# Performance work log

Measured on AMD Instinct MI355X. Metric: run time of the kernel, lower is better.

## Reference

```python
import jax, jax.numpy as jnp
import numpy as np

KS = 10       # kernel_size
OUT_N = 10    # pred_frames_num
DCT_N = 10
BN_INV = 1.0 / np.sqrt(1.0 + 1e-5)  # BN eval with running_mean=0, running_var=1


def _get_dct_matrix(N):
    k = np.arange(N)[:, None].astype(np.float64)
    i = np.arange(N)[None, :].astype(np.float64)
    w = np.full((N, 1), np.sqrt(2.0 / N))
    w[0, 0] = np.sqrt(1.0 / N)
    dct_m = w * np.cos(np.pi * (i + 0.5) * k / N)
    idct_m = np.linalg.inv(dct_m)
    return dct_m.astype(np.float32), idct_m.astype(np.float32)


def _conv1d(x, w):
    # x: [B, Cin, L], w: [Cout, Cin, K] -> [B, Cout, L-K+1]
    return jax.lax.conv_general_dilated(x, w, (1,), 'VALID',
                                        dimension_numbers=('NCH', 'OIH', 'NCH'))


def setup_inputs() -> dict:
    keys = iter(jax.random.split(jax.random.key(0), 32))
    def rn(shape, s=0.06):
        return (jax.random.normal(next(keys), shape, jnp.float32) * s)
    d = {}
    d['src'] = jax.random.normal(next(keys), (128, 50, 66), jnp.float32)
    d['convQ_w1'] = rn((256, 66, 6)); d['convQ_w2'] = rn((256, 256, 5))
    d['convK_w1'] = rn((256, 66, 6)); d['convK_w2'] = rn((256, 256, 5))
    d['gc1_w'] = rn((20, 256)); d['gc1_att'] = rn((66, 66)); d['gc1_b'] = rn((256,))
    d['bn1_g'] = 1.0 + rn((16896,), 0.1); d['bn1_b'] = rn((16896,), 0.1)
    d['gcb_w1'] = rn((12, 256, 256)); d['gcb_att1'] = rn((12, 66, 66)); d['gcb_b1'] = rn((12, 256))
    d['gcb_bn1_g'] = 1.0 + rn((12, 16896), 0.1); d['gcb_bn1_b'] = rn((12, 16896), 0.1)
    d['gcb_w2'] = rn((12, 256, 256)); d['gcb_att2'] = rn((12, 66, 66)); d['gcb_b2'] = rn((12, 256))
    d['gcb_bn2_g'] = 1.0 + rn((12, 16896), 0.1); d['gcb_bn2_b'] = rn((12, 16896), 0.1)
    d['gc7_w'] = rn((256, 20)); d['gc7_att'] = rn((66, 66)); d['gc7_b'] = rn((20,))
    return d


def reference(src, convQ_w1, convQ_w2, convK_w1, convK_w2,
              gc1_w, gc1_att, gc1_b, bn1_g, bn1_b,
              gcb_w1, gcb_att1, gcb_b1, gcb_bn1_g, gcb_bn1_b,
              gcb_w2, gcb_att2, gcb_b2, gcb_bn2_g, gcb_bn2_b,
              gc7_w, gc7_att, gc7_b):
    bs, input_n, F = src.shape  # [128, 50, 66]
    dct_np, idct_np = _get_dct_matrix(KS + OUT_N)
    dct_m = jnp.asarray(dct_np)
    idct_m = jnp.asarray(idct_np)

    src_t = jnp.transpose(src, (0, 2, 1))             # [bs, F, T]
    src_key = src_t[:, :, :input_n - OUT_N]           # [bs, F, 40]
    src_query = src_t[:, :, -KS:]                     # [bs, F, 10]

    vn = input_n - KS - OUT_N + 1                     # 31
    vl = KS + OUT_N                                   # 20
    idx = np.arange(vl)[None, :] + np.arange(vn)[:, None]   # [vn, vl]
    src_value = src[:, idx].reshape(bs * vn, vl, F)   # sliding windows
    src_value = jnp.matmul(dct_m[:DCT_N], src_value)  # [bs*vn, 10, F]
    src_value = src_value.reshape(bs, vn, DCT_N, F).transpose(0, 1, 3, 2).reshape(bs, vn, F * DCT_N)

    key = jax.nn.relu(_conv1d(jax.nn.relu(_conv1d(src_key / 1000.0, convK_w1)), convK_w2))    # [bs,256,31]
    query = jax.nn.relu(_conv1d(jax.nn.relu(_conv1d(src_query / 1000.0, convQ_w1)), convQ_w2))  # [bs,256,1]

    score = jnp.matmul(query.transpose(0, 2, 1), key) + 1e-15   # [bs,1,31]
    att = score / jnp.sum(score, axis=2, keepdims=True)
    dct_att = jnp.matmul(att, src_value)[:, 0].reshape(bs, F, DCT_N)  # [bs,66,10]

    idx2 = np.concatenate([np.arange(input_n - KS, input_n), np.full(OUT_N, input_n - 1)])
    input_gcn = src[:, idx2]                                   # [bs,20,66]
    dct_in = jnp.matmul(dct_m[:DCT_N], input_gcn).transpose(0, 2, 1)  # [bs,66,10]
    x = jnp.concatenate([dct_in, dct_att], axis=-1)            # [bs,66,20]

    def gconv(h, A, W, b):
        # support = h @ W ; out = A @ support + b
        return jnp.einsum('nm,bmf->bnf', A, h @ W) + b

    def bn(h, g, b):
        sh = h.shape
        return (h.reshape(sh[0], -1) * (g * BN_INV) + b).reshape(sh)

    y = jnp.tanh(bn(gconv(x, gc1_att, gc1_w, gc1_b), bn1_g, bn1_b))  # [bs,66,256]

    def block(y, p):
        w1, a1, b1, g1, be1, w2, a2, b2, g2, be2 = p
        h = jnp.tanh(bn(gconv(y, a1, w1, b1), g1, be1))
        h = jnp.tanh(bn(gconv(h, a2, w2, b2), g2, be2))
        return h + y, None

    y, _ = jax.lax.scan(block, y, (gcb_w1, gcb_att1, gcb_b1, gcb_bn1_g, gcb_bn1_b,
                                   gcb_w2, gcb_att2, gcb_b2, gcb_bn2_g, gcb_bn2_b))

    y = gconv(y, gc7_att, gc7_w, gc7_b) + x                    # [bs,66,20]
    out_gcn = jnp.matmul(idct_m[:, :DCT_N], y[:, :, :DCT_N].transpose(0, 2, 1))  # [bs,20,66]
    return out_gcn[:, :, None, :]                              # [bs,20,1,66] (itera=1)
```

## Files before the change

kernel.cpp:

```cpp
#include <hip/hip_runtime.h>
#include <hip/hip_bf16.h>


typedef __attribute__((ext_vector_type(8))) short short8;
typedef __attribute__((ext_vector_type(4))) float float4v;
typedef __attribute__((ext_vector_type(4))) unsigned uint4v;

#define BNI 0.9999950000374995f

__device__ __forceinline__ short f2bf(float x){
  unsigned u = __float_as_uint(x);
  unsigned r = (u + 0x7fff + ((u >> 16) & 1)) >> 16;
  return (short)r;
}
__device__ __forceinline__ unsigned pk2(float a, float b){
  return (unsigned)(unsigned short)f2bf(a) | ((unsigned)(unsigned short)f2bf(b) << 16);
}
__device__ __forceinline__ float tanh_f(float x){
  x = fminf(fmaxf(x, -9.f), 9.f);
  float e = __expf(2.f * x);
  return (e - 1.f) * __builtin_amdgcn_rcpf(e + 1.f);
}

__global__ __launch_bounds__(256) void k_prep(
    const float* __restrict__ wK1, const float* __restrict__ wQ1,
    const float* __restrict__ wK2, const float* __restrict__ wQ2,
    const float* __restrict__ gw1, const float* __restrict__ gw2,
    const float* __restrict__ gc1_w,
    const float* __restrict__ gc1_att, const float* __restrict__ att1,
    const float* __restrict__ att2, const float* __restrict__ gc7_att,
    const float* __restrict__ g0, const float* __restrict__ be0, const float* __restrict__ b0,
    const float* __restrict__ g1a, const float* __restrict__ be1a, const float* __restrict__ b1a,
    const float* __restrict__ g2a, const float* __restrict__ be2a, const float* __restrict__ b2a,
    float* __restrict__ dct, short* __restrict__ w1T, short* __restrict__ w2T,
    short* __restrict__ wgT, short* __restrict__ gc1wT, short* __restrict__ aG,
    unsigned* __restrict__ bnP)
{
  __shared__ short tle[64][72];
  int bid = blockIdx.x, tid = threadIdx.x;
  if (bid < 2){
    int t = bid*256 + tid;
    if (t < 400){
      int k = t / 20, i = t % 20;
      double w = (k == 0) ? sqrt(1.0/20.0) : sqrt(2.0/20.0);
      dct[t] = (float)(w * cos(3.14159265358979323846 * (i + 0.5) * k / 20.0));
    }
  } else if (bid < 1026){
    int idx = (bid-2)*256 + tid;
    int f = idx >> 9, k = idx & 511;
    float v = 0.f;
    if (k < 396){
      int h = k / 66, c = k - h*66;
      const float* s = (f < 256) ? wK1 : wQ1;
      v = s[((f & 255)*66 + c)*6 + h];
    }
    w1T[idx] = f2bf(v);
  } else if (bid < 3586){
    int idx = (bid-1026)*256 + tid;
    int f = idx / 1280, k = idx - f*1280;
    int h = k >> 8, c = k & 255;
    const float* s = (f < 256) ? wK2 : wQ2;
    w2T[idx] = f2bf(s[((f & 255)*256 + c)*5 + h]);
  } else if (bid < 3970){
    int q = bid - 3586;
    int l = q >> 4, sub = q & 15;
    int kt = (sub >> 2)*64, ft = (sub & 3)*64;
    const float* s = (l < 12) ? (gw1 + l*65536) : (gw2 + (l-12)*65536);
    int c = tid & 63, r4 = tid >> 6;
    #pragma unroll
    for (int p = 0; p < 16; p++){
      int k = p*4 + r4;
      tle[k][c] = f2bf(s[(kt + k)*256 + ft + c]);
    }
    __syncthreads();
    #pragma unroll
    for (int p = 0; p < 16; p++){
      int f = p*4 + r4;
      wgT[l*65536 + (ft + f)*256 + kt + c] = tle[c][f];
    }
  } else if (bid < 4002){
    int idx = (bid-3970)*256 + tid;
    int f = idx >> 5, k = idx & 31;
    gc1wT[idx] = f2bf(k < 20 ? gc1_w[k*256 + f] : 0.f);
  } else if (bid < 4782){
    int idx = (bid-4002)*256 + tid;
    int li = idx / 7680, r = idx - li*7680;
    int n = r / 96, m = r - n*96;
    const float* Af;
    if (li == 0) Af = gc1_att;
    else if (li == 25) Af = gc7_att;
    else if (li & 1) Af = att1 + ((li-1)>>1)*4356;
    else             Af = att2 + ((li-2)>>1)*4356;
    aG[idx] = f2bf((n < 66 && m < 66) ? Af[n*66 + m] : 0.f);
  } else {
    int idx = (bid-4782)*256 + tid;
    if (idx < 25*16896){
      int li = idx / 16896, r = idx - li*16896;
      int f = r & 255;
      const float *g, *be, *bi;
      if (li == 0){ g = g0; be = be0; bi = b0; }
      else {
        int l = (li - 1) >> 1;
        if (li & 1){ g = g1a + l*16896; be = be1a + l*16896; bi = b1a + l*256; }
        else       { g = g2a + l*16896; be = be2a + l*16896; bi = b2a + l*256; }
      }
      float sc = g[r] * BNI;
      float sh = bi[f] * sc + be[r];
      bnP[idx] = pk2(sc, sh);
    }
  }
}

__global__ __launch_bounds__(256) void k_conv1(const float* __restrict__ src,
    const short* __restrict__ w1T, short* __restrict__ kc1q){
  int b = blockIdx.x, ns = blockIdx.y;
  int f0 = ns*128;
  __shared__ short Aim[48*424];
  __shared__ short Wt[128*72];
  int tid = threadIdx.x;
  for (int idx = tid; idx < 48*424; idx += 256){
    int t = idx / 424, kk = idx - t*424;
    float v = 0.f;
    if (kk < 396 && t < 40){
      int h = kk / 66, c = kk - h*66;
      int row = t + h + ((t >= 35) ? 5 : 0);
      v = src[(b*50 + row)*66 + c] * 1e-3f;
    }
    Aim[idx] = f2bf(v);
  }
  int w = tid >> 6, lane = tid & 63, fl = lane & 15, g = lane >> 4;
  float4v acc[3][2];
  #pragma unroll
  for (int i=0;i<3;i++) for (int n=0;n<2;n++) acc[i][n] = (float4v){0.f,0.f,0.f,0.f};
  for (int kt = 0; kt < 416; kt += 64){
    __syncthreads();
    for (int ch = tid; ch < 128*8; ch += 256){
      int r = ch >> 3, kq = ch & 7;
      *(short8*)&Wt[r*72 + kq*8] = *(const short8*)&w1T[(f0 + r)*512 + kt + kq*8];
    }
    __syncthreads();
    int nst = (416 - kt >= 64) ? 2 : 1;
    for (int s = 0; s < nst; s++){
      int k0 = s*32;
      short8 bfr0 = *(const short8*)&Wt[(w*32 + fl)*72 + k0 + g*8];
      short8 bfr1 = *(const short8*)&Wt[(w*32 + 16 + fl)*72 + k0 + g*8];
      #pragma unroll
      for (int i=0;i<3;i++){
        short8 afr = *(const short8*)&Aim[(i*16 + fl)*424 + kt + k0 + g*8];
        acc[i][0] = __builtin_amdgcn_mfma_f32_16x16x32_bf16(afr, bfr0, acc[i][0], 0,0,0);
        acc[i][1] = __builtin_amdgcn_mfma_f32_16x16x32_bf16(afr, bfr1, acc[i][1], 0,0,0);
      }
    }
  }
  #pragma unroll
  for (int i=0;i<3;i++) for (int n=0;n<2;n++) for (int j=0;j<4;j++){
    int t = i*16 + g*4 + j;
    int f = f0 + w*32 + n*16 + fl;
    float v = fmaxf(acc[i][n][j], 0.f);
    if (t < 35 && f < 256) kc1q[(b*40 + t)*256 + f] = f2bf(v);
    else if (t >= 35 && t < 40 && f >= 256) kc1q[(b*40 + t)*256 + (f - 256)] = f2bf(v);
  }
}

__global__ __launch_bounds__(256) void k_conv2(const short* __restrict__ kc1q,
    const short* __restrict__ w2T, float* __restrict__ key, float* __restrict__ q){
  int b = blockIdx.x, ns = blockIdx.y;
  int f0 = ns*128;
  __shared__ short kcs[40*256];
  __shared__ short Wt[128*136];
  char* kcb = (char*)kcs;
  int tid = threadIdx.x;
  for (int ch = tid; ch < 1280; ch += 256){
    int r = ch >> 5, kq = ch & 31;
    unsigned byte = (unsigned)(r*512 + kq*16) ^ (unsigned)((r & 7) << 4);
    *(short8*)(kcb + byte) = *(const short8*)&kc1q[(b*40 + r)*256 + kq*8];
  }
  int w = tid >> 6, lane = tid & 63, fl = lane & 15, g = lane >> 4;
  float4v acc[2][2];
  #pragma unroll
  for (int i=0;i<2;i++) for (int n=0;n<2;n++) acc[i][n] = (float4v){0.f,0.f,0.f,0.f};
  for (int kt = 0; kt < 1280; kt += 128){
    __syncthreads();
    for (int ch = tid; ch < 128*16; ch += 256){
      int r = ch >> 4, kq = ch & 15;
      *(short8*)&Wt[r*136 + kq*8] = *(const short8*)&w2T[(f0 + r)*1280 + kt + kq*8];
    }
    __syncthreads();
    #pragma unroll
    for (int s = 0; s < 4; s++){
      int k = kt + s*32;
      int h = k >> 8, cb = k & 255;
      short8 bfr0 = *(const short8*)&Wt[(w*32 + fl)*136 + s*32 + g*8];
      short8 bfr1 = *(const short8*)&Wt[(w*32 + 16 + fl)*136 + s*32 + g*8];
      #pragma unroll
      for (int i=0;i<2;i++){
        int t = i*16 + fl;
        int row = t + h + ((t == 31) ? 4 : 0);
        unsigned byte = (unsigned)(row*512 + (cb + g*8)*2) ^ (unsigned)((row & 7) << 4);
        short8 afr = *(const short8*)(kcb + byte);
        acc[i][0] = __builtin_amdgcn_mfma_f32_16x16x32_bf16(afr, bfr0, acc[i][0], 0,0,0);
        acc[i][1] = __builtin_amdgcn_mfma_f32_16x16x32_bf16(afr, bfr1, acc[i][1], 0,0,0);
      }
    }
  }
  #pragma unroll
  for (int i=0;i<2;i++) for (int n=0;n<2;n++) for (int j=0;j<4;j++){
    int t = i*16 + g*4 + j;
    int f = f0 + w*32 + n*16 + fl;
    float v = fmaxf(acc[i][n][j], 0.f);
    if (t < 31 && f < 256) key[(b*31 + t)*256 + f] = v;
    else if (t == 31 && f >= 256) q[b*256 + f - 256] = v;
  }
}

__global__ __launch_bounds__(256) void k_attx(const float* __restrict__ src,
    const float* __restrict__ q, const float* __restrict__ key,
    const float* __restrict__ dct, float* __restrict__ x, short* __restrict__ x_bf){
  int b = blockIdx.x;
  int tid = threadIdx.x;
  __shared__ float sred[31][9];
  __shared__ float a[31];
  __shared__ float z[20*66];
  for (int i = tid; i < 2560; i += 256) x_bf[b*2560 + i] = 0;
  if (tid < 248){
    int v = tid >> 3, p = tid & 7;
    const float* kr = key + (b*31 + v)*256 + p*32;
    const float* qr = q + b*256 + p*32;
    float s = 0.f;
    #pragma unroll
    for (int o = 0; o < 32; o++) s += qr[o] * kr[o];
    sred[v][p] = s;
  }
  __syncthreads();
  if (tid < 31){
    float s = 1e-15f;
    #pragma unroll
    for (int p = 0; p < 8; p++) s += sred[tid][p];
    sred[tid][8] = s;
  }
  __syncthreads();
  if (tid < 64){
    float v = (tid < 31) ? sred[tid][8] : 0.f;
    float tot = v;
    for (int off = 32; off; off >>= 1) tot += __shfl_down(tot, off);
    tot = __shfl(tot, 0);
    if (tid < 31) a[tid] = v / tot;
  }
  __syncthreads();
  for (int idx = tid; idx < 1320; idx += 256){
    int i = idx / 66, f = idx % 66;
    float s = 0.f;
    for (int v = 0; v < 31; v++) s += a[v] * src[(b*50 + v + i)*66 + f];
    z[idx] = s;
  }
  __syncthreads();
  for (int idx = tid; idx < 660; idx += 256){
    int f = idx / 10, k = idx % 10;
    float s1 = 0.f, s2 = 0.f;
    #pragma unroll
    for (int i = 0; i < 20; i++){
      float d = dct[k*20 + i];
      int tt = (i < 10) ? (40 + i) : 49;
      s1 += d * src[(b*50 + tt)*66 + f];
      s2 += d * z[i*66 + f];
    }
    x[(b*66 + f)*20 + k] = s1;
    x[(b*66 + f)*20 + 10 + k] = s2;
    x_bf[(b*80 + f)*32 + k] = f2bf(s1);
    x_bf[(b*80 + f)*32 + 10 + k] = f2bf(s2);
  }
}


template<int KSTEPS, int KSTRIDE, int MODE>
__device__ __forceinline__ void layer_step(
    const short* __restrict__ Wg,
    const unsigned* __restrict__ bnl, const short* __restrict__ aGl,
    float4v (&y_r)[2][5], int w, int fl, int g,
    const char* __restrict__ yin, char* __restrict__ yout, char* __restrict__ tT_c)
{
  const short* wbase = Wg + (w*32 + fl)*KSTRIDE + g*8;
  short8 bw[3][2];
  bw[0][0] = *(const short8*)(wbase);
  bw[0][1] = *(const short8*)(wbase + 16*KSTRIDE);
  if (KSTEPS > 1){
    bw[1][0] = *(const short8*)(wbase + 32);
    bw[1][1] = *(const short8*)(wbase + 16*KSTRIDE + 32);
  }
  short8 bA[15];
  #pragma unroll
  for (int ks=0;ks<3;ks++)
    #pragma unroll
    for (int n2=0;n2<5;n2++)
      bA[ks*5+n2] = *(const short8*)&aGl[(n2*16 + fl)*96 + ks*32 + g*8];

  float4v acc[5][2];
  #pragma unroll
  for (int i=0;i<5;i++){ acc[i][0]=(float4v){0.f,0.f,0.f,0.f}; acc[i][1]=(float4v){0.f,0.f,0.f,0.f}; }
  #pragma unroll
  for (int ks=0; ks<KSTEPS; ks++){
    if (ks + 2 < KSTEPS){
      bw[(ks+2)%3][0] = *(const short8*)(wbase + (ks+2)*32);
      bw[(ks+2)%3][1] = *(const short8*)(wbase + 16*KSTRIDE + (ks+2)*32);
    }
    #pragma unroll
    for (int i=0;i<5;i++){
      int m = i*16 + fl;
      short8 af = *(const short8*)(yin + m*512 + ((ks*64 + g*16) ^ ((m & 15) << 4)));
      acc[i][0] = __builtin_amdgcn_mfma_f32_16x16x32_bf16(af, bw[ks%3][0], acc[i][0], 0,0,0);
      acc[i][1] = __builtin_amdgcn_mfma_f32_16x16x32_bf16(af, bw[ks%3][1], acc[i][1], 0,0,0);
    }
  }
  #pragma unroll
  for (int i=0;i<5;i++){
    int mb = (i*16 + g*4)*2;
    #pragma unroll
    for (int n=0;n<2;n++){
      int f = w*32 + n*16 + fl;
      uint2 u; u.x = pk2(acc[i][n][0], acc[i][n][1]); u.y = pk2(acc[i][n][2], acc[i][n][3]);
      *(uint2*)(tT_c + f*256 + (mb ^ ((f & 15) << 4))) = u;
    }
  }

  uint4v bnp0[5], bnp1[5];
  #pragma unroll
  for (int n2=0;n2<5;n2++){
    int n = n2*16 + fl; int ns = (n < 66) ? n : 0;
    bnp0[n2] = *(const uint4v*)&bnl[ns*256 + w*32 + g*4];
  }
  float4v a2[2][5];
  #pragma unroll
  for (int i=0;i<2;i++)
    #pragma unroll
    for (int n=0;n<5;n++) a2[i][n] = (float4v){0.f,0.f,0.f,0.f};

#define G2STEP(ks) { \
    _Pragma("unroll") \
    for (int i2=0;i2<2;i2++){ \
      int f = w*32 + i2*16 + fl; \
      short8 af = *(const short8*)(tT_c + f*256 + (((ks)*64 + g*16) ^ ((f & 15) << 4))); \
      _Pragma("unroll") \
      for (int n2=0;n2<5;n2++) \
        a2[i2][n2] = __builtin_amdgcn_mfma_f32_16x16x32_bf16(af, bA[(ks)*5+n2], a2[i2][n2], 0,0,0); \
    } }

  G2STEP(0)
  #pragma unroll
  for (int n2=0;n2<5;n2++){
    int n = n2*16 + fl; int ns = (n < 66) ? n : 0;
    bnp1[n2] = *(const uint4v*)&bnl[ns*256 + w*32 + 16 + g*4];
  }
  G2STEP(1)
  G2STEP(2)
#undef G2STEP

  #pragma unroll
  for (int i2=0;i2<2;i2++){
    #pragma unroll
    for (int n2=0;n2<5;n2++){
      int n = n2*16 + fl;
      bool nok = (n < 66);
      float vv[4];
      #pragma unroll
      for (int j=0;j<4;j++){
        unsigned u = (i2 == 0) ? bnp0[n2][j] : bnp1[n2][j];
        float sc = __uint_as_float((u & 0xffffu) << 16);
        float sh = __uint_as_float(u & 0xffff0000u);
        float v = a2[i2][n2][j]*sc + sh;
        v = tanh_f(v);
        if (MODE == 0) y_r[i2][n2][j] = v;
        if (MODE == 2){ v += y_r[i2][n2][j]; y_r[i2][n2][j] = v; }
        vv[j] = nok ? v : 0.f;
      }
      int fb2 = (w*32 + i2*16 + g*4)*2;
      uint2 u2; u2.x = pk2(vv[0], vv[1]); u2.y = pk2(vv[2], vv[3]);
      *(uint2*)(yout + n*512 + (fb2 ^ ((n & 15) << 4))) = u2;
    }
  }
  __syncthreads();
}

__global__ __launch_bounds__(512) void k_mega(const short* __restrict__ x_bf,
    const short* __restrict__ gc1wT, const short* __restrict__ wgT,
    const short* __restrict__ aG, const unsigned* __restrict__ bnP,
    const float* __restrict__ gc7_w, const float* __restrict__ gc7_b,
    const float* __restrict__ x, const float* __restrict__ dct,
    float* __restrict__ out)
{
  __shared__ __align__(16) char ybf_c[81920];
  __shared__ __align__(16) char tT_c[65536];
  __shared__ float xo_l[1320];
  __shared__ float dct_l[400];

  int b = blockIdx.x, tid = threadIdx.x;
  int w = tid >> 6, lane = tid & 63, fl = lane & 15, g = lane >> 4;
  char* ybf0 = ybf_c;
  char* ybf1 = ybf_c + 40960;

  for (int i = tid; i < 400; i += 512) dct_l[i] = dct[i];
  for (int i = tid; i < 320; i += 512){
    int m = i >> 2, kq = i & 3;
    short8 v = *(const short8*)&x_bf[(b*80 + m)*32 + kq*8];
    *(short8*)(ybf0 + m*512 + ((kq*16) ^ ((m & 15) << 4))) = v;
  }
  __syncthreads();

  float4v y_r[2][5];

  layer_step<1,32,0>(gc1wT, bnP, aG, y_r, w, fl, g, ybf0, ybf1, tT_c);
  for (int l = 0; l < 12; l++){
    layer_step<8,256,1>(wgT + l*65536, bnP + (1+2*l)*16896, aG + (1+2*l)*7680,
                        y_r, w, fl, g, ybf1, ybf0, tT_c);
    layer_step<8,256,2>(wgT + (12+l)*65536, bnP + (2+2*l)*16896, aG + (2+2*l)*7680,
                        y_r, w, fl, g, ybf0, ybf1, tT_c);
  }

  for (int i = tid; i < 2048; i += 512){
    int f = i >> 6, kq = (i & 63)*4;
    float v0=0.f, v1=0.f, v2=0.f, v3=0.f;
    if (f < 20){
      v0 = gc7_w[(kq+0)*20 + f]; v1 = gc7_w[(kq+1)*20 + f];
      v2 = gc7_w[(kq+2)*20 + f]; v3 = gc7_w[(kq+3)*20 + f];
    }
    uint2 u; u.x = pk2(v0, v1); u.y = pk2(v2, v3);
    *(uint2*)(ybf0 + f*512 + ((kq*2) ^ ((f & 15) << 4))) = u;
  }
  short8 bAt[15];
  {
    const short* aGt = aG + 25*7680;
    #pragma unroll
    for (int ks=0;ks<3;ks++)
      #pragma unroll
      for (int n2=0;n2<5;n2++)
        bAt[ks*5+n2] = *(const short8*)&aGt[(n2*16 + fl)*96 + ks*32 + g*8];
  }
  __syncthreads();

  float4v at[5][2];
  #pragma unroll
  for (int i=0;i<5;i++){ at[i][0] = (float4v){0.f,0.f,0.f,0.f}; at[i][1] = (float4v){0.f,0.f,0.f,0.f}; }
  #pragma unroll
  for (int ks = 0; ks < 8; ks++){
    short8 bf[2];
    #pragma unroll
    for (int n=0;n<2;n++){
      int f = n*16 + fl;
      bf[n] = *(const short8*)(ybf0 + f*512 + ((ks*64 + g*16) ^ ((f & 15) << 4)));
    }
    #pragma unroll
    for (int i=0;i<5;i++){
      int m = i*16 + fl;
      short8 af = *(const short8*)(ybf1 + m*512 + ((ks*64 + g*16) ^ ((m & 15) << 4)));
      at[i][0] = __builtin_amdgcn_mfma_f32_16x16x32_bf16(af, bf[0], at[i][0], 0,0,0);
      at[i][1] = __builtin_amdgcn_mfma_f32_16x16x32_bf16(af, bf[1], at[i][1], 0,0,0);
    }
  }
  if (w == 0){
    #pragma unroll
    for (int i=0;i<5;i++){
      int mb = (i*16 + g*4)*2;
      #pragma unroll
      for (int n=0;n<2;n++){
        int f = n*16 + fl;
        uint2 u; u.x = pk2(at[i][n][0], at[i][n][1]); u.y = pk2(at[i][n][2], at[i][n][3]);
        *(uint2*)(tT_c + f*256 + (mb ^ ((f & 15) << 4))) = u;
      }
    }
  }
  __syncthreads();

  float4v a2t[2][5];
  #pragma unroll
  for (int i=0;i<2;i++)
    #pragma unroll
    for (int n=0;n<5;n++) a2t[i][n] = (float4v){0.f,0.f,0.f,0.f};
  #pragma unroll
  for (int ks = 0; ks < 3; ks++){
    #pragma unroll
    for (int i2=0;i2<2;i2++){
      int f = i2*16 + fl;
      short8 af = *(const short8*)(tT_c + f*256 + ((ks*64 + g*16) ^ ((f & 15) << 4)));
      #pragma unroll
      for (int n2=0;n2<5;n2++)
        a2t[i2][n2] = __builtin_amdgcn_mfma_f32_16x16x32_bf16(af, bAt[ks*5+n2], a2t[i2][n2], 0,0,0);
    }
  }
  if (w == 0){
    #pragma unroll
    for (int i2=0;i2<2;i2++){
      #pragma unroll
      for (int n2=0;n2<5;n2++){
        int n = n2*16 + fl;
        #pragma unroll
        for (int j=0;j<4;j++){
          int f = i2*16 + g*4 + j;
          if (f < 20 && n < 66)
            xo_l[n*20 + f] = a2t[i2][n2][j] + gc7_b[f] + x[(b*66 + n)*20 + f];
        }
      }
    }
  }
  __syncthreads();

  for (int idx = tid; idx < 1320; idx += 512){
    int r = idx / 66, fn = idx % 66;
    float s = 0.f;
    #pragma unroll
    for (int k = 0; k < 10; k++) s += dct_l[k*20 + r] * xo_l[fn*20 + k];
    out[(b*20 + r)*66 + fn] = s;
  }
}

extern "C" void kernel_launch(void* const* d_in, const int* in_sizes, int n_in,
                              void* d_out, int out_size, void* d_ws, size_t ws_size,
                              hipStream_t stream) {
  const float* src      = (const float*)d_in[0];
  const float* convQ_w1 = (const float*)d_in[1];
  const float* convQ_w2 = (const float*)d_in[2];
  const float* convK_w1 = (const float*)d_in[3];
  const float* convK_w2 = (const float*)d_in[4];
  const float* gc1_w    = (const float*)d_in[5];
  const float* gc1_att  = (const float*)d_in[6];
  const float* gc1_b    = (const float*)d_in[7];
  const float* bn1_g    = (const float*)d_in[8];
  const float* bn1_b    = (const float*)d_in[9];
  const float* gcb_w1   = (const float*)d_in[10];
  const float* gcb_att1 = (const float*)d_in[11];
  const float* gcb_b1   = (const float*)d_in[12];
  const float* gcb_bn1g = (const float*)d_in[13];
  const float* gcb_bn1b = (const float*)d_in[14];
  const float* gcb_w2   = (const float*)d_in[15];
  const float* gcb_att2 = (const float*)d_in[16];
  const float* gcb_b2   = (const float*)d_in[17];
  const float* gcb_bn2g = (const float*)d_in[18];
  const float* gcb_bn2b = (const float*)d_in[19];
  const float* gc7_w    = (const float*)d_in[20];
  const float* gc7_att  = (const float*)d_in[21];
  const float* gc7_b    = (const float*)d_in[22];
  float* out = (float*)d_out;

  float* ws    = (float*)d_ws;
  float* dct   = ws;
  float* x     = ws + 512;
  short* x_bf  = (short*)(ws + 169472);
  short* wgT   = (short*)(ws + 333312);
  short* gc1wT = (short*)(ws + 1119744);
  short* w1T   = (short*)(ws + 1123840);
  short* w2T   = (short*)(ws + 1254912);
  short* kc1q  = (short*)(ws + 1582592);
  float* key   = ws + 2237952;
  float* q     = ws + 3253760;
  unsigned* bnP= (unsigned*)(ws + 3290624);
  short* aG    = (short*)(ws + 3713024);

  k_prep<<<6432, 256, 0, stream>>>(convK_w1, convQ_w1, convK_w2, convQ_w2,
      gcb_w1, gcb_w2, gc1_w,
      gc1_att, gcb_att1, gcb_att2, gc7_att,
      bn1_g, bn1_b, gc1_b, gcb_bn1g, gcb_bn1b, gcb_b1,
      gcb_bn2g, gcb_bn2b, gcb_b2,
      dct, w1T, w2T, wgT, gc1wT, aG, bnP);

  k_conv1<<<dim3(128,4), 256, 0, stream>>>(src, w1T, kc1q);
  k_conv2<<<dim3(128,4), 256, 0, stream>>>(kc1q, w2T, key, q);
  k_attx<<<128, 256, 0, stream>>>(src, q, key, dct, x, x_bf);

  k_mega<<<128, 512, 0, stream>>>(x_bf, gc1wT, wgT, aG, bnP,
      gc7_w, gc7_b, x, dct, out);
}
```

Baseline: 328.8 us.

## Split the mega-kernel GCN layers across 16 waves with 16 features each

```diff
diff --git a/kernel.cpp b/kernel.cpp
--- a/kernel.cpp
+++ b/kernel.cpp
@@ -276,111 +276,101 @@
 __device__ __forceinline__ void layer_step(
     const short* __restrict__ Wg,
     const unsigned* __restrict__ bnl, const short* __restrict__ aGl,
-    float4v (&y_r)[2][5], int w, int fl, int g,
+    float4v (&y_r)[5], int w, int fl, int g,
     const char* __restrict__ yin, char* __restrict__ yout, char* __restrict__ tT_c)
 {
-  const short* wbase = Wg + (w*32 + fl)*KSTRIDE + g*8;
-  short8 bw[3][2];
-  bw[0][0] = *(const short8*)(wbase);
-  bw[0][1] = *(const short8*)(wbase + 16*KSTRIDE);
-  if (KSTEPS > 1){
-    bw[1][0] = *(const short8*)(wbase + 32);
-    bw[1][1] = *(const short8*)(wbase + 16*KSTRIDE + 32);
-  }
-  short8 bA[15];
-  #pragma unroll
-  for (int ks=0;ks<3;ks++)
-    #pragma unroll
-    for (int n2=0;n2<5;n2++)
-      bA[ks*5+n2] = *(const short8*)&aGl[(n2*16 + fl)*96 + ks*32 + g*8];
-
-  float4v acc[5][2];
-  #pragma unroll
-  for (int i=0;i<5;i++){ acc[i][0]=(float4v){0.f,0.f,0.f,0.f}; acc[i][1]=(float4v){0.f,0.f,0.f,0.f}; }
+  const short* wbase = Wg + (w*16 + fl)*KSTRIDE + g*8;
+  short8 bw[3];
+  bw[0] = *(const short8*)(wbase);
+  if (KSTEPS > 1) bw[1] = *(const short8*)(wbase + 32);
+  short8 bA0[5], bA1[5];
+  #pragma unroll
+  for (int n2=0;n2<5;n2++)
+    bA0[n2] = *(const short8*)&aGl[(n2*16 + fl)*96 + g*8];
+
+  float4v acc[5];
+  #pragma unroll
+  for (int i=0;i<5;i++) acc[i] = (float4v){0.f,0.f,0.f,0.f};
   #pragma unroll
   for (int ks=0; ks<KSTEPS; ks++){
-    if (ks + 2 < KSTEPS){
-      bw[(ks+2)%3][0] = *(const short8*)(wbase + (ks+2)*32);
-      bw[(ks+2)%3][1] = *(const short8*)(wbase + 16*KSTRIDE + (ks+2)*32);
-    }
+    if (ks + 2 < KSTEPS) bw[(ks+2)%3] = *(const short8*)(wbase + (ks+2)*32);
     #pragma unroll
     for (int i=0;i<5;i++){
       int m = i*16 + fl;
       short8 af = *(const short8*)(yin + m*512 + ((ks*64 + g*16) ^ ((m & 15) << 4)));
-      acc[i][0] = __builtin_amdgcn_mfma_f32_16x16x32_bf16(af, bw[ks%3][0], acc[i][0], 0,0,0);
-      acc[i][1] = __builtin_amdgcn_mfma_f32_16x16x32_bf16(af, bw[ks%3][1], acc[i][1], 0,0,0);
-    }
-  }
-  #pragma unroll
-  for (int i=0;i<5;i++){
-    int mb = (i*16 + g*4)*2;
-    #pragma unroll
-    for (int n=0;n<2;n++){
-      int f = w*32 + n*16 + fl;
-      uint2 u; u.x = pk2(acc[i][n][0], acc[i][n][1]); u.y = pk2(acc[i][n][2], acc[i][n][3]);
+      acc[i] = __builtin_amdgcn_mfma_f32_16x16x32_bf16(af, bw[ks%3], acc[i], 0,0,0);
+    }
+  }
+  {
+    int f = w*16 + fl;
+    #pragma unroll
+    for (int i=0;i<5;i++){
+      int mb = (i*16 + g*4)*2;
+      uint2 u; u.x = pk2(acc[i][0], acc[i][1]); u.y = pk2(acc[i][2], acc[i][3]);
       *(uint2*)(tT_c + f*256 + (mb ^ ((f & 15) << 4))) = u;
     }
   }
 
-  uint4v bnp0[5], bnp1[5];
+  float4v a2[5];
+  #pragma unroll
+  for (int n2=0;n2<5;n2++) a2[n2] = (float4v){0.f,0.f,0.f,0.f};
+  int f = w*16 + fl;
+
+  #pragma unroll
+  for (int n2=0;n2<5;n2++)
+    bA1[n2] = *(const short8*)&aGl[(n2*16 + fl)*96 + 32 + g*8];
+  {
+    short8 af = *(const short8*)(tT_c + f*256 + ((g*16) ^ ((f & 15) << 4)));
+    #pragma unroll
+    for (int n2=0;n2<5;n2++)
+      a2[n2] = __builtin_amdgcn_mfma_f32_16x16x32_bf16(af, bA0[n2], a2[n2], 0,0,0);
+  }
+  #pragma unroll
+  for (int n2=0;n2<5;n2++)
+    bA0[n2] = *(const short8*)&aGl[(n2*16 + fl)*96 + 64 + g*8];
+  {
+    short8 af = *(const short8*)(tT_c + f*256 + ((64 + g*16) ^ ((f & 15) << 4)));
+    #pragma unroll
+    for (int n2=0;n2<5;n2++)
+      a2[n2] = __builtin_amdgcn_mfma_f32_16x16x32_bf16(af, bA1[n2], a2[n2], 0,0,0);
+  }
+  uint4v bnp[5];
   #pragma unroll
   for (int n2=0;n2<5;n2++){
     int n = n2*16 + fl; int ns = (n < 66) ? n : 0;
-    bnp0[n2] = *(const uint4v*)&bnl[ns*256 + w*32 + g*4];
-  }
-  float4v a2[2][5];
-  #pragma unroll
-  for (int i=0;i<2;i++)
-    #pragma unroll
-    for (int n=0;n<5;n++) a2[i][n] = (float4v){0.f,0.f,0.f,0.f};
-
-#define G2STEP(ks) { \
-    _Pragma("unroll") \
-    for (int i2=0;i2<2;i2++){ \
-      int f = w*32 + i2*16 + fl; \
-      short8 af = *(const short8*)(tT_c + f*256 + (((ks)*64 + g*16) ^ ((f & 15) << 4))); \
-      _Pragma("unroll") \
-      for (int n2=0;n2<5;n2++) \
-        a2[i2][n2] = __builtin_amdgcn_mfma_f32_16x16x32_bf16(af, bA[(ks)*5+n2], a2[i2][n2], 0,0,0); \
-    } }
-
-  G2STEP(0)
+    bnp[n2] = *(const uint4v*)&bnl[ns*256 + w*16 + g*4];
+  }
+  {
+    short8 af = *(const short8*)(tT_c + f*256 + ((128 + g*16) ^ ((f & 15) << 4)));
+    #pragma unroll
+    for (int n2=0;n2<5;n2++)
+      a2[n2] = __builtin_amdgcn_mfma_f32_16x16x32_bf16(af, bA0[n2], a2[n2], 0,0,0);
+  }
+
   #pragma unroll
   for (int n2=0;n2<5;n2++){
-    int n = n2*16 + fl; int ns = (n < 66) ? n : 0;
-    bnp1[n2] = *(const uint4v*)&bnl[ns*256 + w*32 + 16 + g*4];
-  }
-  G2STEP(1)
-  G2STEP(2)
-#undef G2STEP
-
-  #pragma unroll
-  for (int i2=0;i2<2;i2++){
-    #pragma unroll
-    for (int n2=0;n2<5;n2++){
-      int n = n2*16 + fl;
-      bool nok = (n < 66);
-      float vv[4];
-      #pragma unroll
-      for (int j=0;j<4;j++){
-        unsigned u = (i2 == 0) ? bnp0[n2][j] : bnp1[n2][j];
-        float sc = __uint_as_float((u & 0xffffu) << 16);
-        float sh = __uint_as_float(u & 0xffff0000u);
-        float v = a2[i2][n2][j]*sc + sh;
-        v = tanh_f(v);
-        if (MODE == 0) y_r[i2][n2][j] = v;
-        if (MODE == 2){ v += y_r[i2][n2][j]; y_r[i2][n2][j] = v; }
-        vv[j] = nok ? v : 0.f;
-      }
-      int fb2 = (w*32 + i2*16 + g*4)*2;
-      uint2 u2; u2.x = pk2(vv[0], vv[1]); u2.y = pk2(vv[2], vv[3]);
-      *(uint2*)(yout + n*512 + (fb2 ^ ((n & 15) << 4))) = u2;
-    }
-  }
-  __syncthreads();
-}
-
-__global__ __launch_bounds__(512) void k_mega(const short* __restrict__ x_bf,
+    int n = n2*16 + fl;
+    bool nok = (n < 66);
+    float vv[4];
+    #pragma unroll
+    for (int j=0;j<4;j++){
+      unsigned u = bnp[n2][j];
+      float sc = __uint_as_float((u & 0xffffu) << 16);
+      float sh = __uint_as_float(u & 0xffff0000u);
+      float v = a2[n2][j]*sc + sh;
+      v = tanh_f(v);
+      if (MODE == 0) y_r[n2][j] = v;
+      if (MODE == 2){ v += y_r[n2][j]; y_r[n2][j] = v; }
+      vv[j] = nok ? v : 0.f;
+    }
+    int fb2 = (w*16 + g*4)*2;
+    uint2 u2; u2.x = pk2(vv[0], vv[1]); u2.y = pk2(vv[2], vv[3]);
+    *(uint2*)(yout + n*512 + (fb2 ^ ((n & 15) << 4))) = u2;
+  }
+  __syncthreads();
+}
+
+__global__ __launch_bounds__(1024) void k_mega(const short* __restrict__ x_bf,
     const short* __restrict__ gc1wT, const short* __restrict__ wgT,
     const short* __restrict__ aG, const unsigned* __restrict__ bnP,
     const float* __restrict__ gc7_w, const float* __restrict__ gc7_b,
@@ -397,15 +387,15 @@
   char* ybf0 = ybf_c;
   char* ybf1 = ybf_c + 40960;
 
-  for (int i = tid; i < 400; i += 512) dct_l[i] = dct[i];
-  for (int i = tid; i < 320; i += 512){
+  for (int i = tid; i < 400; i += 1024) dct_l[i] = dct[i];
+  for (int i = tid; i < 320; i += 1024){
     int m = i >> 2, kq = i & 3;
     short8 v = *(const short8*)&x_bf[(b*80 + m)*32 + kq*8];
     *(short8*)(ybf0 + m*512 + ((kq*16) ^ ((m & 15) << 4))) = v;
   }
   __syncthreads();
 
-  float4v y_r[2][5];
+  float4v y_r[5];
 
   layer_step<1,32,0>(gc1wT, bnP, aG, y_r, w, fl, g, ybf0, ybf1, tT_c);
   for (int l = 0; l < 12; l++){
@@ -415,7 +405,7 @@
                         y_r, w, fl, g, ybf0, ybf1, tT_c);
   }
 
-  for (int i = tid; i < 2048; i += 512){
+  for (int i = tid; i < 2048; i += 1024){
     int f = i >> 6, kq = (i & 63)*4;
     float v0=0.f, v1=0.f, v2=0.f, v3=0.f;
     if (f < 20){
@@ -502,7 +492,7 @@
   }
   __syncthreads();
 
-  for (int idx = tid; idx < 1320; idx += 512){
+  for (int idx = tid; idx < 1320; idx += 1024){
     int r = idx / 66, fn = idx % 66;
     float s = 0.f;
     #pragma unroll
@@ -564,6 +554,6 @@
   k_conv2<<<dim3(128,4), 256, 0, stream>>>(kc1q, w2T, key, q);
   k_attx<<<128, 256, 0, stream>>>(src, q, key, dct, x, x_bf);
 
-  k_mega<<<128, 512, 0, stream>>>(x_bf, gc1wT, wgT, aG, bnP,
+  k_mega<<<128, 1024, 0, stream>>>(x_bf, gc1wT, wgT, aG, bnP,
       gc7_w, gc7_b, x, dct, out);
 }
```

After: 367.8 us. 11.9% more time.

## Stream adjacency fragments per k-step, add MFMA priority hints, use hardware bf16 pack

Applied to the files above, without the earlier changes.

```diff
diff --git a/kernel.cpp b/kernel.cpp
--- a/kernel.cpp
+++ b/kernel.cpp
@@ -14,7 +14,9 @@
   return (short)r;
 }
 __device__ __forceinline__ unsigned pk2(float a, float b){
-  return (unsigned)(unsigned short)f2bf(a) | ((unsigned)(unsigned short)f2bf(b) << 16);
+  unsigned r;
+  asm("v_cvt_pk_bf16_f32 %0, %1, %2" : "=v"(r) : "v"(a), "v"(b));
+  return r;
 }
 __device__ __forceinline__ float tanh_f(float x){
   x = fminf(fmaxf(x, -9.f), 9.f);
@@ -277,7 +279,8 @@
     const short* __restrict__ Wg,
     const unsigned* __restrict__ bnl, const short* __restrict__ aGl,
     float4v (&y_r)[2][5], int w, int fl, int g,
-    const char* __restrict__ yin, char* __restrict__ yout, char* __restrict__ tT_c)
+    const char* __restrict__ yin, char* __restrict__ yout,
+    char* __restrict__ tT_c)
 {
   const short* wbase = Wg + (w*32 + fl)*KSTRIDE + g*8;
   short8 bw[3][2];
@@ -287,16 +290,11 @@
     bw[1][0] = *(const short8*)(wbase + 32);
     bw[1][1] = *(const short8*)(wbase + 16*KSTRIDE + 32);
   }
-  short8 bA[15];
-  #pragma unroll
-  for (int ks=0;ks<3;ks++)
-    #pragma unroll
-    for (int n2=0;n2<5;n2++)
-      bA[ks*5+n2] = *(const short8*)&aGl[(n2*16 + fl)*96 + ks*32 + g*8];
 
   float4v acc[5][2];
   #pragma unroll
   for (int i=0;i<5;i++){ acc[i][0]=(float4v){0.f,0.f,0.f,0.f}; acc[i][1]=(float4v){0.f,0.f,0.f,0.f}; }
+  __builtin_amdgcn_s_setprio(1);
   #pragma unroll
   for (int ks=0; ks<KSTEPS; ks++){
     if (ks + 2 < KSTEPS){
@@ -311,6 +309,13 @@
       acc[i][1] = __builtin_amdgcn_mfma_f32_16x16x32_bf16(af, bw[ks%3][1], acc[i][1], 0,0,0);
     }
   }
+  __builtin_amdgcn_s_setprio(0);
+
+  short8 bA[5];
+  #pragma unroll
+  for (int n2=0;n2<5;n2++)
+    bA[n2] = *(const short8*)&aGl[(n2*16 + fl)*96 + g*8];
+
   #pragma unroll
   for (int i=0;i<5;i++){
     int mb = (i*16 + g*4)*2;
@@ -322,38 +327,44 @@
     }
   }
 
-  uint4v bnp0[5], bnp1[5];
-  #pragma unroll
-  for (int n2=0;n2<5;n2++){
-    int n = n2*16 + fl; int ns = (n < 66) ? n : 0;
-    bnp0[n2] = *(const uint4v*)&bnl[ns*256 + w*32 + g*4];
-  }
   float4v a2[2][5];
   #pragma unroll
   for (int i=0;i<2;i++)
     #pragma unroll
     for (int n=0;n<5;n++) a2[i][n] = (float4v){0.f,0.f,0.f,0.f};
-
-#define G2STEP(ks) { \
-    _Pragma("unroll") \
-    for (int i2=0;i2<2;i2++){ \
-      int f = w*32 + i2*16 + fl; \
-      short8 af = *(const short8*)(tT_c + f*256 + (((ks)*64 + g*16) ^ ((f & 15) << 4))); \
-      _Pragma("unroll") \
-      for (int n2=0;n2<5;n2++) \
-        a2[i2][n2] = __builtin_amdgcn_mfma_f32_16x16x32_bf16(af, bA[(ks)*5+n2], a2[i2][n2], 0,0,0); \
-    } }
-
-  G2STEP(0)
+  uint4v bnp0[5];
+  #pragma unroll
+  for (int ks2=0; ks2<3; ks2++){
+    __builtin_amdgcn_s_setprio(1);
+    #pragma unroll
+    for (int i2=0;i2<2;i2++){
+      int f = w*32 + i2*16 + fl;
+      short8 af = *(const short8*)(tT_c + f*256 + ((ks2*64 + g*16) ^ ((f & 15) << 4)));
+      #pragma unroll
+      for (int n2=0;n2<5;n2++)
+        a2[i2][n2] = __builtin_amdgcn_mfma_f32_16x16x32_bf16(af, bA[n2], a2[i2][n2], 0,0,0);
+    }
+    __builtin_amdgcn_s_setprio(0);
+    if (ks2 == 1){
+      #pragma unroll
+      for (int n2=0;n2<5;n2++){
+        int n = n2*16 + fl; int ns = (n < 66) ? n : 0;
+        bnp0[n2] = *(const uint4v*)&bnl[ns*256 + w*32 + g*4];
+      }
+    }
+    if (ks2 < 2){
+      #pragma unroll
+      for (int n2=0;n2<5;n2++)
+        bA[n2] = *(const short8*)&aGl[(n2*16 + fl)*96 + (ks2+1)*32 + g*8];
+    }
+  }
+
+  uint4v bnp1[5];
   #pragma unroll
   for (int n2=0;n2<5;n2++){
     int n = n2*16 + fl; int ns = (n < 66) ? n : 0;
     bnp1[n2] = *(const uint4v*)&bnl[ns*256 + w*32 + 16 + g*4];
   }
-  G2STEP(1)
-  G2STEP(2)
-#undef G2STEP
-
   #pragma unroll
   for (int i2=0;i2<2;i2++){
     #pragma unroll
@@ -397,6 +408,7 @@
   char* ybf0 = ybf_c;
   char* ybf1 = ybf_c + 40960;
 
+  for (int i = tid; i < 4096; i += 512) ((float4v*)tT_c)[i] = (float4v){0.f,0.f,0.f,0.f};
   for (int i = tid; i < 400; i += 512) dct_l[i] = dct[i];
   for (int i = tid; i < 320; i += 512){
     int m = i >> 2, kq = i & 3;
@@ -425,15 +437,6 @@
     uint2 u; u.x = pk2(v0, v1); u.y = pk2(v2, v3);
     *(uint2*)(ybf0 + f*512 + ((kq*2) ^ ((f & 15) << 4))) = u;
   }
-  short8 bAt[15];
-  {
-    const short* aGt = aG + 25*7680;
-    #pragma unroll
-    for (int ks=0;ks<3;ks++)
-      #pragma unroll
-      for (int n2=0;n2<5;n2++)
-        bAt[ks*5+n2] = *(const short8*)&aGt[(n2*16 + fl)*96 + ks*32 + g*8];
-  }
   __syncthreads();
 
   float4v at[5][2];
@@ -466,6 +469,15 @@
         *(uint2*)(tT_c + f*256 + (mb ^ ((f & 15) << 4))) = u;
       }
     }
+  }
+  short8 bAt[15];
+  {
+    const short* aGt = aG + 25*7680;
+    #pragma unroll
+    for (int ks=0;ks<3;ks++)
+      #pragma unroll
+      for (int n2=0;n2<5;n2++)
+        bAt[ks*5+n2] = *(const short8*)&aGt[(n2*16 + fl)*96 + ks*32 + g*8];
   }
   __syncthreads();
 
```

Measured after the change: 290.5 us. 1.13x faster.
